# Kernel optimization log

Measured on AMD Instinct MI355X. Metric: run time of the kernel, lower is better.

Reference implementation:

```python
import jax, jax.numpy as jnp
import numpy as np

B, S, C = 32, 128, 32
VOCAB, E, H = 262, 128, 256


def _gru_dir(x_proj, mask, W_hh, b_hh, reverse):
    # x_proj: [C, N, 3H] time-major precomputed input projection
    # mask:   [C, N, 1]  1.0 where char is valid
    N = x_proj.shape[1]
    h0 = jnp.zeros((N, H), x_proj.dtype)

    def step(h, inp):
        x3, mt = inp
        gh = h @ W_hh.T + b_hh                      # [N, 3H]
        hr, hz, hn = jnp.split(gh, 3, axis=-1)
        xr, xz, xn = jnp.split(x3, 3, axis=-1)
        r = jax.nn.sigmoid(xr + hr)
        z = jax.nn.sigmoid(xz + hz)
        n = jnp.tanh(xn + r * hn)
        hnew = (1.0 - z) * n + z * h
        h = mt * hnew + (1.0 - mt) * h              # freeze state past seq end
        return h, None

    hT, _ = jax.lax.scan(step, h0, (x_proj, mask), reverse=reverse)
    return hT  # [N, H] final state at last valid step (fw) / step 0 (bw)


def char_rnn_forward(chars, chars_mask, data_mask, embed,
                     W_ih_fw, W_hh_fw, b_ih_fw, b_hh_fw,
                     W_ih_bw, W_hh_bw, b_ih_bw, b_hh_bw):
    b, s, c = chars.shape
    N = b * s
    x = embed[chars.reshape(N, c)]                      # [N, C, E]
    m = chars_mask.reshape(N, c).astype(x.dtype)        # [N, C]
    mm = jnp.moveaxis(m, 1, 0)[:, :, None]              # [C, N, 1]

    def run(W_ih, b_ih, W_hh, b_hh, reverse):
        xp = jnp.einsum('nce,ge->ncg', x, W_ih) + b_ih  # [N, C, 3H]
        xp = jnp.moveaxis(xp, 1, 0)                     # [C, N, 3H]
        return _gru_dir(xp, mm, W_hh, b_hh, reverse)

    h_fw = run(W_ih_fw, b_ih_fw, W_hh_fw, b_hh_fw, False)
    h_bw = run(W_ih_bw, b_ih_bw, W_hh_bw, b_hh_bw, True)
    final = jnp.concatenate([h_fw, h_bw], axis=-1).reshape(b, s, 2 * H)
    return final * data_mask[:, :, None].astype(final.dtype)


def setup_inputs() -> dict:
    key = jax.random.key(0)
    ks = jax.random.split(key, 16)
    chars = jax.random.randint(ks[0], (B, S, C), 0, VOCAB, dtype=jnp.int32)
    # ragged but contiguous lengths, as pack_padded_sequence assumes (>=1)
    word_len = jax.random.randint(ks[1], (B,), 1, S + 1)
    char_len = jax.random.randint(ks[2], (B, S), 1, C + 1)
    data_mask = (jnp.arange(S)[None, :] < word_len[:, None]).astype(jnp.int32)
    chars_mask = (jnp.arange(C)[None, None, :] < char_len[:, :, None]).astype(jnp.int32)
    chars_mask = chars_mask * data_mask[:, :, None]
    # pack_padded needs length>=1 even for padded words (torch never runs them;
    # we mask their output with data_mask, so give them 1 valid char)
    chars_mask = chars_mask.at[:, :, 0].set(1)

    sc = 1.0 / np.sqrt(H)
    def unif(k, shape):
        return jax.random.uniform(k, shape, jnp.float32, -sc, sc)
    embed = jax.random.normal(ks[3], (VOCAB, E), jnp.float32) * 0.1
    return {
        'chars': chars, 'chars_mask': chars_mask, 'data_mask': data_mask,
        'embed': embed,
        'W_ih_fw': unif(ks[4], (3 * H, E)), 'W_hh_fw': unif(ks[5], (3 * H, H)),
        'b_ih_fw': unif(ks[6], (3 * H,)),  'b_hh_fw': unif(ks[7], (3 * H,)),
        'W_ih_bw': unif(ks[8], (3 * H, E)), 'W_hh_bw': unif(ks[9], (3 * H, H)),
        'b_ih_bw': unif(ks[10], (3 * H,)), 'b_hh_bw': unif(ks[11], (3 * H,)),
    }


def reference(chars, chars_mask, data_mask, embed,
              W_ih_fw, W_hh_fw, b_ih_fw, b_hh_fw,
              W_ih_bw, W_hh_bw, b_ih_bw, b_hh_bw):
    return char_rnn_forward(chars, chars_mask, data_mask, embed,
                            W_ih_fw, W_hh_fw, b_ih_fw, b_hh_fw,
                            W_ih_bw, W_hh_bw, b_ih_bw, b_hh_bw)
```

## Files before the change

kernel.cpp:

```cpp
#include <hip/hip_runtime.h>
#include <hip/hip_bf16.h>

typedef unsigned int u32;
typedef unsigned short u16;
typedef __attribute__((ext_vector_type(8))) short bf16x8;
typedef __attribute__((ext_vector_type(4))) float f32x4;

#define NWORDS 4096
#define CC 32
#define EE 128
#define HHH 256
#define MMW 32
#define VOCABN 262

#define HS 264
#define XPS 784

#define PK_HHD (16*3*8*512)
#define XP_OFF_U16 (2*PK_HHD)
#define XPD (VOCABN*768)
#define BIAS_OFF_U16 (XP_OFF_U16 + 2*XPD)

#define XP_NCH 8
#define XP_CBLK ((VOCABN + XP_NCH - 1) / XP_NCH)
#define PREP_PACK_BLKS (2*PK_HHD/256)
#define PREP_XP_BLKS (XP_CBLK*2)
#define PREP_BLKS (PREP_PACK_BLKS + PREP_XP_BLKS + 1)

__device__ __forceinline__ float bf2f(u16 u){ union{u32 i; float f;} v; v.i=((u32)u)<<16; return v.f; }
__device__ __forceinline__ u16 f2bf(float f){
  __hip_bfloat16 h = __float2bfloat16(f);
  u16 r; __builtin_memcpy(&r, &h, 2); return r;
}
__device__ __forceinline__ float sigmoid_f(float x){
  float e = __builtin_amdgcn_exp2f(-1.4426950408889634f * x);
  return __builtin_amdgcn_rcpf(1.0f + e);
}
__device__ __forceinline__ float tanh_f(float x){
  float ax = __builtin_fabsf(x);
  float e  = __builtin_amdgcn_exp2f(-2.8853900817779268f * ax);
  float t  = 1.0f - 2.0f * e * __builtin_amdgcn_rcpf(1.0f + e);
  return __builtin_copysignf(t, x);
}

__global__ void prep_all(const float* __restrict__ emb,
                         const float* __restrict__ Wih_fw, const float* __restrict__ Whh_fw,
                         const float* __restrict__ bih_fw, const float* __restrict__ bhh_fw,
                         const float* __restrict__ Wih_bw, const float* __restrict__ Whh_bw,
                         const float* __restrict__ bih_bw, const float* __restrict__ bhh_bw,
                         u16* __restrict__ wsu)
{
  const int bid = blockIdx.x, tid = threadIdx.x;
  if (bid < PREP_PACK_BLKS) {
    int idx = bid*256 + tid;
    int d = idx / PK_HHD;
    int e = idx - d*PK_HHD;
    const float* Whh = d ? Whh_bw : Whh_fw;
    int jj   = e & 7;
    int lane = (e >> 3) & 63;
    int kc   = (e >> 9) & 7;
    int gnt  = e >> 12;
    int g = gnt % 3, nt = gnt / 3;
    int row = g*256 + nt*16 + (lane & 15);
    int k   = kc*32 + ((lane >> 4) << 3) + jj;
    wsu[idx] = f2bf(Whh[row*HHH + k]);
  } else if (bid < PREP_PACK_BLKS + PREP_XP_BLKS) {
    const int b    = bid - PREP_PACK_BLKS;
    const int dirb = b & 1;
    const int c0   = (b >> 1) * XP_NCH;
    const float* Wih = dirb ? Wih_bw : Wih_fw;
    u16* xpo = wsu + XP_OFF_U16 + (size_t)dirb*XPD;

    __shared__ float sh_E[XP_NCH][EE];
    for (int i = tid; i < XP_NCH*EE; i += 256) {
      int c = c0 + i/EE;
      sh_E[0][i] = (c < VOCABN) ? emb[(size_t)c*EE + (i & (EE-1))] : 0.0f;
    }
    __syncthreads();

    #pragma unroll 1
    for (int q = 0; q < 3; ++q) {
      const int g = q*256 + tid;
      const float* W = Wih + (size_t)g*EE;
      float acc[XP_NCH];
      #pragma unroll
      for (int c = 0; c < XP_NCH; ++c) acc[c] = 0.0f;
      #pragma unroll 2
      for (int k = 0; k < EE; k += 4) {
        float4 wv = *(const float4*)(W + k);
        #pragma unroll
        for (int c = 0; c < XP_NCH; ++c) {
          float4 ev = *(const float4*)(&sh_E[c][k]);
          acc[c] = fmaf(ev.w, wv.w, fmaf(ev.z, wv.z, fmaf(ev.y, wv.y, fmaf(ev.x, wv.x, acc[c]))));
        }
      }
      #pragma unroll
      for (int c = 0; c < XP_NCH; ++c) {
        int ci = c0 + c;
        if (ci < VOCABN) xpo[(size_t)ci*768 + g] = f2bf(acc[c]);
      }
    }
  } else {
    #pragma unroll
    for (int rep = 0; rep < 8; ++rep) {
      int i = rep*256 + tid;
      int d = i >> 10, o = i & 1023;
      const float* bih = d ? bih_bw : bih_fw;
      const float* bhh = d ? bhh_bw : bhh_fw;
      float v;
      if (o < 512)      v = bih[o] + bhh[o];
      else if (o < 768) v = bih[o - 512 + 512];
      else              v = bhh[o - 768 + 512];
      ((float*)(wsu + BIAS_OFF_U16))[d*1024 + o] = v;
    }
  }
}

__global__ __launch_bounds__(1024)
void gru_mfma(const int* __restrict__ chars, const int* __restrict__ chars_mask,
              const int* __restrict__ data_mask, const u16* __restrict__ wsu,
              float* __restrict__ out)
{
  const int dir   = blockIdx.x & 1;
  const int word0 = (blockIdx.x >> 1) * MMW;
  const int j     = threadIdx.x;
  const int wave  = j >> 6, lane = j & 63;
  const int quad  = lane >> 4, l15 = lane & 15;

  const bf16x8* pHH  = (const bf16x8*)(wsu + (size_t)dir*PK_HHD);
  const u16*    xpt  = wsu + XP_OFF_U16 + (size_t)dir*XPD;
  const float*  bias = (const float*)(wsu + BIAS_OFF_U16) + dir*1024;

  const bf16x8* bHH = pHH + (size_t)(wave*3)*8*64 + lane;

  __shared__ __align__(16) u16   sh_hhi[MMW][HS];
  __shared__ __align__(16) u16   sh_hlo[MMW][HS];
  __shared__ __align__(16) u16   sh_xp[MMW][XPS];
  __shared__ int   sh_ci[MMW][CC + 1];
  __shared__ float sh_cm[MMW][CC + 1];

  {
    const int w = j >> 5, c = j & 31;
    sh_ci[w][c] = chars[(word0 + w)*CC + c];
    sh_cm[w][c] = (float)chars_mask[(word0 + w)*CC + c];
  }
  for (int i = j; i < MMW*HS/2; i += 1024) { ((float*)sh_hhi)[i] = 0.0f; ((float*)sh_hlo)[i] = 0.0f; }

  const int ch = wave*16 + l15;
  const float bR  = bias[ch],        bZ  = bias[256 + ch];
  const float bXN = bias[512 + ch],  bHN = bias[768 + ch];

  const int sw = j >> 5, sp = j & 31;

  bf16x8 buf[4][3];
  auto load_batch = [&](int kc, bf16x8 dst[3]) {
    #pragma unroll
    for (int g = 0; g < 3; ++g) dst[g] = bHH[(g*8 + kc)*64];
  };
  load_batch(0, buf[0]);
  load_batch(1, buf[1]);
  load_batch(2, buf[2]);

  #pragma unroll 1
  for (int s = 0; s < CC; ++s) {
    const int t = dir ? (CC - 1 - s) : s;
    __syncthreads();
    {
      int ci = sh_ci[sw][t];
      const uint4* src = (const uint4*)(xpt + (size_t)ci*768);
      uint4 a0 = src[sp*3], a1 = src[sp*3+1], a2 = src[sp*3+2];
      *(uint4*)&sh_xp[sw][sp*24]      = a0;
      *(uint4*)&sh_xp[sw][sp*24 + 8]  = a1;
      *(uint4*)&sh_xp[sw][sp*24 + 16] = a2;
    }

    f32x4 acc[3][2];
    #pragma unroll
    for (int m = 0; m < 2; ++m) {
      acc[0][m] = (f32x4){bR,bR,bR,bR};
      acc[1][m] = (f32x4){bZ,bZ,bZ,bZ};
      acc[2][m] = (f32x4){bHN,bHN,bHN,bHN};
    }

    auto mfma_batch = [&](int kc, bf16x8 src[3]) {
      #pragma unroll
      for (int m = 0; m < 2; ++m) {
        bf16x8 ah = *(const bf16x8*)&sh_hhi[m*16 + l15][kc*32 + quad*8];
        bf16x8 al = *(const bf16x8*)&sh_hlo[m*16 + l15][kc*32 + quad*8];
        acc[0][m] = __builtin_amdgcn_mfma_f32_16x16x32_bf16(ah, src[0], acc[0][m], 0,0,0);
        acc[1][m] = __builtin_amdgcn_mfma_f32_16x16x32_bf16(ah, src[1], acc[1][m], 0,0,0);
        acc[2][m] = __builtin_amdgcn_mfma_f32_16x16x32_bf16(ah, src[2], acc[2][m], 0,0,0);
        acc[2][m] = __builtin_amdgcn_mfma_f32_16x16x32_bf16(al, src[2], acc[2][m], 0,0,0);
      }
    };

    #pragma unroll
    for (int b = 0; b < 8; ++b) {
      mfma_batch(b, buf[b & 3]);
      load_batch((b + 3) & 7, buf[(b + 3) & 3]);
    }

    __syncthreads();

    #pragma unroll
    for (int m = 0; m < 2; ++m)
      #pragma unroll
      for (int r = 0; r < 4; ++r) {
        const int word = m*16 + quad*4 + r;
        float xr = bf2f(sh_xp[word][ch]);
        float xz = bf2f(sh_xp[word][256 + ch]);
        float xn = bf2f(sh_xp[word][512 + ch]);
        float rr = sigmoid_f(acc[0][m][r] + xr);
        float zz = sigmoid_f(acc[1][m][r] + xz);
        float nn = tanh_f(fmaf(rr, acc[2][m][r], bXN + xn));
        float hold = bf2f(sh_hhi[word][ch]) + bf2f(sh_hlo[word][ch]);
        float hnew = fmaf(zz, hold - nn, nn);
        float hm   = fmaf(sh_cm[word][t], hnew - hold, hold);
        u16 hi = f2bf(hm);
        sh_hhi[word][ch] = hi;
        sh_hlo[word][ch] = f2bf(hm - bf2f(hi));
      }
  }
  __syncthreads();

  const int oc = j & 255, og = j >> 8;
  #pragma unroll
  for (int i = 0; i < 8; ++i) {
    const int w = og*8 + i;
    float dm = (float)data_mask[word0 + w];
    float h = bf2f(sh_hhi[w][oc]) + bf2f(sh_hlo[w][oc]);
    out[(size_t)(word0 + w)*(2*HHH) + dir*HHH + oc] = h * dm;
  }
}

extern "C" void kernel_launch(void* const* d_in, const int* in_sizes, int n_in,
                              void* d_out, int out_size, void* d_ws, size_t ws_size,
                              hipStream_t stream) {
  const int*   chars      = (const int*)d_in[0];
  const int*   chars_mask = (const int*)d_in[1];
  const int*   data_mask  = (const int*)d_in[2];
  const float* embed      = (const float*)d_in[3];
  const float* Wih_fw     = (const float*)d_in[4];
  const float* Whh_fw     = (const float*)d_in[5];
  const float* bih_fw     = (const float*)d_in[6];
  const float* bhh_fw     = (const float*)d_in[7];
  const float* Wih_bw     = (const float*)d_in[8];
  const float* Whh_bw     = (const float*)d_in[9];
  const float* bih_bw     = (const float*)d_in[10];
  const float* bhh_bw     = (const float*)d_in[11];
  u16* wsu = (u16*)d_ws;

  prep_all<<<PREP_BLKS, 256, 0, stream>>>(embed, Wih_fw, Whh_fw, bih_fw, bhh_fw,
                                          Wih_bw, Whh_bw, bih_bw, bhh_bw, wsu);

  gru_mfma<<<(NWORDS/MMW)*2, 1024, 0, stream>>>(chars, chars_mask, data_mask, wsu, (float*)d_out);
}
```

Measured before the change: 354.6 us.

## Load per-lane input projections directly into registers, keep hidden state in registers

Re-lays the precomputed vocab×gate projection table so each hidden channel's r,z (bf16) and n (fp32) values sit contiguously in 8 bytes. Each lane then gathers its own projection values straight from global/L2 into registers before the barrier, replacing the cooperative staging through shared memory. The change also keeps the fp32 hidden state in registers, packs the char mask into ballot bitmasks, and writes the output from registers. This removes a large shared-memory buffer and its store/load traffic per step. In exchange it adds eight small scattered global loads per lane per step, plus a larger workspace table.

```diff
diff --git a/kernel.cpp b/kernel.cpp
--- a/kernel.cpp
+++ b/kernel.cpp
@@ -3,6 +3,7 @@
 
 typedef unsigned int u32;
 typedef unsigned short u16;
+typedef unsigned long long u64;
 typedef __attribute__((ext_vector_type(8))) short bf16x8;
 typedef __attribute__((ext_vector_type(4))) float f32x4;
 
@@ -14,11 +15,10 @@
 #define VOCABN 262
 
 #define HS 264
-#define XPS 784
 
 #define PK_HHD (16*3*8*512)
 #define XP_OFF_U16 (2*PK_HHD)
-#define XPD (VOCABN*768)
+#define XPD (VOCABN*1024)
 #define BIAS_OFF_U16 (XP_OFF_U16 + 2*XPD)
 
 #define XP_NCH 8
@@ -97,7 +97,10 @@
       #pragma unroll
       for (int c = 0; c < XP_NCH; ++c) {
         int ci = c0 + c;
-        if (ci < VOCABN) xpo[(size_t)ci*768 + g] = f2bf(acc[c]);
+        if (ci < VOCABN) {
+          if (q < 2) xpo[(size_t)ci*1024 + tid*4 + q] = f2bf(acc[c]);
+          else ((float*)xpo)[(size_t)ci*512 + tid*2 + 1] = acc[c];
+        }
       }
     }
   } else {
@@ -133,24 +136,37 @@
 
   const bf16x8* bHH = pHH + (size_t)(wave*3)*8*64 + lane;
 
-  __shared__ __align__(16) u16   sh_hhi[MMW][HS];
-  __shared__ __align__(16) u16   sh_hlo[MMW][HS];
-  __shared__ __align__(16) u16   sh_xp[MMW][XPS];
-  __shared__ int   sh_ci[MMW][CC + 1];
-  __shared__ float sh_cm[MMW][CC + 1];
+  __shared__ __align__(16) u16 sh_hhi[MMW][HS];
+  __shared__ __align__(16) u16 sh_hlo[MMW][HS];
+  __shared__ __align__(16) int sh_cit[CC][MMW];
+  __shared__ u32 sh_mb[MMW];
 
   {
     const int w = j >> 5, c = j & 31;
-    sh_ci[w][c] = chars[(word0 + w)*CC + c];
-    sh_cm[w][c] = (float)chars_mask[(word0 + w)*CC + c];
+    sh_cit[c][w] = chars[(word0 + w)*CC + c];
+    int mv = chars_mask[(word0 + w)*CC + c];
+    u64 bal = __ballot(mv != 0);
+    if (lane == 0) {
+      sh_mb[2*wave]     = (u32)bal;
+      sh_mb[2*wave + 1] = (u32)(bal >> 32);
+    }
   }
   for (int i = j; i < MMW*HS/2; i += 1024) { ((float*)sh_hhi)[i] = 0.0f; ((float*)sh_hlo)[i] = 0.0f; }
+  __syncthreads();
 
   const int ch = wave*16 + l15;
   const float bR  = bias[ch],        bZ  = bias[256 + ch];
   const float bXN = bias[512 + ch],  bHN = bias[768 + ch];
 
-  const int sw = j >> 5, sp = j & 31;
+  u32 mb[2][4];
+  float hreg[2][4];
+  #pragma unroll
+  for (int m = 0; m < 2; ++m)
+    #pragma unroll
+    for (int r = 0; r < 4; ++r) {
+      mb[m][r] = sh_mb[m*16 + quad*4 + r];
+      hreg[m][r] = 0.0f;
+    }
 
   bf16x8 buf[4][3];
   auto load_batch = [&](int kc, bf16x8 dst[3]) {
@@ -164,15 +180,23 @@
   #pragma unroll 1
   for (int s = 0; s < CC; ++s) {
     const int t = dir ? (CC - 1 - s) : s;
+
+    uint2 xv[2][4];
+    {
+      int4 ciA = *(const int4*)&sh_cit[t][quad*4];
+      int4 ciB = *(const int4*)&sh_cit[t][16 + quad*4];
+      const u16* xb = xpt + (size_t)ch*4;
+      xv[0][0] = *(const uint2*)(xb + (size_t)ciA.x*1024);
+      xv[0][1] = *(const uint2*)(xb + (size_t)ciA.y*1024);
+      xv[0][2] = *(const uint2*)(xb + (size_t)ciA.z*1024);
+      xv[0][3] = *(const uint2*)(xb + (size_t)ciA.w*1024);
+      xv[1][0] = *(const uint2*)(xb + (size_t)ciB.x*1024);
+      xv[1][1] = *(const uint2*)(xb + (size_t)ciB.y*1024);
+      xv[1][2] = *(const uint2*)(xb + (size_t)ciB.z*1024);
+      xv[1][3] = *(const uint2*)(xb + (size_t)ciB.w*1024);
+    }
+
     __syncthreads();
-    {
-      int ci = sh_ci[sw][t];
-      const uint4* src = (const uint4*)(xpt + (size_t)ci*768);
-      uint4 a0 = src[sp*3], a1 = src[sp*3+1], a2 = src[sp*3+2];
-      *(uint4*)&sh_xp[sw][sp*24]      = a0;
-      *(uint4*)&sh_xp[sw][sp*24 + 8]  = a1;
-      *(uint4*)&sh_xp[sw][sp*24 + 16] = a2;
-    }
 
     f32x4 acc[3][2];
     #pragma unroll
@@ -207,30 +231,32 @@
       #pragma unroll
       for (int r = 0; r < 4; ++r) {
         const int word = m*16 + quad*4 + r;
-        float xr = bf2f(sh_xp[word][ch]);
-        float xz = bf2f(sh_xp[word][256 + ch]);
-        float xn = bf2f(sh_xp[word][512 + ch]);
+        u32 xw = xv[m][r].x;
+        float xr = bf2f((u16)(xw & 0xffffu));
+        float xz = bf2f((u16)(xw >> 16));
+        union { u32 u; float f; } xnu; xnu.u = xv[m][r].y;
         float rr = sigmoid_f(acc[0][m][r] + xr);
         float zz = sigmoid_f(acc[1][m][r] + xz);
-        float nn = tanh_f(fmaf(rr, acc[2][m][r], bXN + xn));
-        float hold = bf2f(sh_hhi[word][ch]) + bf2f(sh_hlo[word][ch]);
+        float nn = tanh_f(fmaf(rr, acc[2][m][r], bXN + xnu.f));
+        float hold = hreg[m][r];
         float hnew = fmaf(zz, hold - nn, nn);
-        float hm   = fmaf(sh_cm[word][t], hnew - hold, hold);
+        float cmf  = (float)((mb[m][r] >> t) & 1u);
+        float hm   = fmaf(cmf, hnew - hold, hold);
+        hreg[m][r] = hm;
         u16 hi = f2bf(hm);
         sh_hhi[word][ch] = hi;
         sh_hlo[word][ch] = f2bf(hm - bf2f(hi));
       }
   }
-  __syncthreads();
-
-  const int oc = j & 255, og = j >> 8;
+
   #pragma unroll
-  for (int i = 0; i < 8; ++i) {
-    const int w = og*8 + i;
-    float dm = (float)data_mask[word0 + w];
-    float h = bf2f(sh_hhi[w][oc]) + bf2f(sh_hlo[w][oc]);
-    out[(size_t)(word0 + w)*(2*HHH) + dir*HHH + oc] = h * dm;
-  }
+  for (int m = 0; m < 2; ++m)
+    #pragma unroll
+    for (int r = 0; r < 4; ++r) {
+      const int word = m*16 + quad*4 + r;
+      float dm = (float)data_mask[word0 + word];
+      out[(size_t)(word0 + word)*(2*HHH) + dir*HHH + ch] = hreg[m][r] * dm;
+    }
 }
 
 extern "C" void kernel_launch(void* const* d_in, const int* in_sizes, int n_in,
```

Measured after the change: 478.1 us. +34.8%, slower.
